# Performance work log

Measured on AMD Instinct MI355X. Metric: run time of the kernel, lower is better.

The kernel has to match this reference:

```python
import jax, jax.numpy as jnp
import numpy as np

THETA = 10000.0

def apply_rope(x, positions):
    # x: [B, H, S, D_head], positions: [S] int
    d = x.shape[-1]
    inv_freq = THETA ** (-jnp.arange(0, d, 2, dtype=jnp.float32) / d)  # [d/2]
    ang = positions.astype(jnp.float32)[:, None] * inv_freq[None, :]   # [S, d/2]
    cos, sin = jnp.cos(ang), jnp.sin(ang)                              # broadcast over B,H
    x1, x2 = x[..., 0::2], x[..., 1::2]
    r1 = x1 * cos - x2 * sin
    r2 = x1 * sin + x2 * cos
    return jnp.stack([r1, r2], axis=-1).reshape(x.shape)


def setup_inputs() -> dict:
    key = jax.random.key(0)
    ks = jax.random.split(key, 5)
    B, S, D = 4, 2048, 1024
    scale = 1.0 / np.sqrt(D)
    return {
        "x": jax.random.normal(ks[0], (B, S, D), dtype=jnp.float32),
        "Wq": jax.random.normal(ks[1], (D, D), dtype=jnp.float32) * scale,
        "Wk": jax.random.normal(ks[2], (D, D), dtype=jnp.float32) * scale,
        "Wv": jax.random.normal(ks[3], (D, D), dtype=jnp.float32) * scale,
        "Wo": jax.random.normal(ks[4], (D, D), dtype=jnp.float32) * scale,
        "token_positions": jnp.arange(S, dtype=jnp.int32),
    }


def reference(x, Wq, Wk, Wv, Wo, token_positions):
    B, S, D = x.shape
    H = 16
    hd = D // H
    # fused QKV projection (weights stored [out, in], y = x @ W^T, no bias)
    qkv_w = jnp.concatenate([Wq, Wk, Wv], axis=0)          # [3D, D]
    qkv = x @ qkv_w.T                                      # [B, S, 3D]
    q, k, v = jnp.split(qkv, 3, axis=-1)
    # [B, S, D] -> [B, H, S, hd]
    def split_heads(t):
        return t.reshape(B, S, H, hd).transpose(0, 2, 1, 3)
    q, k, v = split_heads(q), split_heads(k), split_heads(v)
    q = apply_rope(q, token_positions)
    k = apply_rope(k, token_positions)
    scores = jnp.einsum('bhqd,bhkd->bhqk', q, k) / jnp.sqrt(jnp.float32(hd))
    causal = jnp.tril(jnp.ones((S, S), dtype=bool))        # True = attend
    scores = jnp.where(causal[None, None], scores, -jnp.inf)
    attn = jax.nn.softmax(scores, axis=-1)
    out = jnp.einsum('bhqk,bhkd->bhqd', attn, v)           # [B, H, S, hd]
    out = out.transpose(0, 2, 1, 3).reshape(B, S, D)
    return out @ Wo.T
```

## Files before the change

### kernel.cpp

```cpp
#include <hip/hip_runtime.h>
#include <hip/hip_bf16.h>


typedef __bf16 bf16x8 __attribute__((ext_vector_type(8)));
typedef float f32x4 __attribute__((ext_vector_type(4)));
typedef unsigned short u16x8 __attribute__((ext_vector_type(8)));

#define DEV static __device__ __forceinline__

DEV unsigned short f2bf(float f) {
  unsigned int u = __builtin_bit_cast(unsigned int, f);
  u += 0x7FFFu + ((u >> 16) & 1u);
  return (unsigned short)(u >> 16);
}
DEV float bf2f(unsigned short h) {
  unsigned int u = ((unsigned int)h) << 16;
  return __builtin_bit_cast(float, u);
}
DEV bf16x8 ld_bf8(const unsigned short* p) {
  union { u16x8 u; bf16x8 b; } c;
  c.u = *reinterpret_cast<const u16x8*>(p);
  return c.b;
}
DEV unsigned int pk2(float a, float b) {
  unsigned int r;
  asm("v_cvt_pk_bf16_f32 %0, %1, %2" : "=v"(r) : "v"(a), "v"(b));
  return r;
}

DEV void gload_lds16(const unsigned short* src, unsigned short* dst) {
  __builtin_amdgcn_global_load_lds(
      (const __attribute__((address_space(1))) void*)src,
      (__attribute__((address_space(3))) void*)dst, 16, 0, 0);
}

DEV void stage_tile(const unsigned short* g, int ldg, unsigned short* lds,
                    int wave, int lane) {
  int rl = lane >> 3;
  int c16 = lane & 7;
#pragma unroll
  for (int i = 0; i < 4; ++i) {
    int row = i * 32 + wave * 8 + rl;
    int sc16 = c16 ^ (row & 7);
    const unsigned short* src = g + (size_t)row * ldg + sc16 * 8;
    unsigned short* dst = lds + (i * 32 + wave * 8) * 64;
    gload_lds16(src, dst);
  }
}

DEV bf16x8 lds_frag(const unsigned short* lds, int row, int c16) {
  return ld_bf8(lds + row * 64 + ((c16 ^ (row & 7)) << 3));
}

__global__ void k_f32_to_bf16(const float* __restrict__ in,
                              unsigned short* __restrict__ out, int n4) {
  int i = blockIdx.x * blockDim.x + threadIdx.x;
  if (i < n4) {
    float4 v = reinterpret_cast<const float4*>(in)[i];
    uint2 o;
    o.x = pk2(v.x, v.y);
    o.y = pk2(v.z, v.w);
    reinterpret_cast<uint2*>(out)[i] = o;
  }
}

__global__ void k_conv_w(const float* __restrict__ Wq, const float* __restrict__ Wk,
                         const float* __restrict__ Wv, const float* __restrict__ Wo,
                         unsigned short* __restrict__ Wb, unsigned short* __restrict__ Wob) {
  int i = blockIdx.x * blockDim.x + threadIdx.x;
  int which = i >> 18, j = i & 262143;
  const float* src = (which == 0) ? Wq : (which == 1) ? Wk : (which == 2) ? Wv : Wo;
  unsigned short* dst = (which == 3) ? Wob : Wb + (size_t)which * 1048576;
  float4 v = reinterpret_cast<const float4*>(src)[j];
  uint2 o;
  o.x = pk2(v.x, v.y);
  o.y = pk2(v.z, v.w);
  reinterpret_cast<uint2*>(dst)[j] = o;
}

__global__ void k_rope_table(const int* __restrict__ pos, float* __restrict__ tab) {
  int idx = blockIdx.x * blockDim.x + threadIdx.x;
  if (idx >= 2048 * 32) return;
  int s = idx >> 5, i = idx & 31;
  double inv = pow(10000.0, -(double)(2 * i) / 64.0);
  double ang = (double)pos[s] * inv;
  tab[idx * 2]     = (float)cos(ang);
  tab[idx * 2 + 1] = (float)sin(ang);
}

__global__ __launch_bounds__(256) void k_gemm_qkv(
    const unsigned short* __restrict__ A, const unsigned short* __restrict__ W,
    unsigned short* __restrict__ Qh, unsigned short* __restrict__ Kh,
    unsigned short* __restrict__ Vt, const float* __restrict__ tab) {
  const int Kd = 1024, S = 2048;
  __shared__ __align__(16) unsigned short As[128 * 64];
  __shared__ __align__(16) unsigned short Bs[128 * 64];
  int m0 = blockIdx.x * 128, n0 = blockIdx.y * 128;
  int wave = threadIdx.x >> 6, lane = threadIdx.x & 63;
  int wm = wave >> 1, wn = wave & 1;
  int lr = lane & 15, lk = lane >> 4;
  const unsigned short* Ag = A + (size_t)m0 * Kd;
  const unsigned short* Wg = W + (size_t)n0 * Kd;
  f32x4 acc[4][4] = {};
  for (int k0 = 0; k0 < Kd; k0 += 64) {
    stage_tile(Ag + k0, Kd, As, wave, lane);
    stage_tile(Wg + k0, Kd, Bs, wave, lane);
    __syncthreads();
#pragma unroll
    for (int ks = 0; ks < 2; ++ks) {
      bf16x8 a[4], b[4];
#pragma unroll
      for (int fm = 0; fm < 4; ++fm) a[fm] = lds_frag(As, wm * 64 + fm * 16 + lr, ks * 4 + lk);
#pragma unroll
      for (int fn = 0; fn < 4; ++fn) b[fn] = lds_frag(Bs, wn * 64 + fn * 16 + lr, ks * 4 + lk);
#pragma unroll
      for (int fm = 0; fm < 4; ++fm)
#pragma unroll
        for (int fn = 0; fn < 4; ++fn)
          acc[fm][fn] = __builtin_amdgcn_mfma_f32_16x16x32_bf16(a[fm], b[fn], acc[fm][fn], 0, 0, 0);
    }
    __syncthreads();
  }
  int t = n0 >> 10;
  if (t == 2) {
#pragma unroll
    for (int fm = 0; fm < 4; ++fm) {
      int row = m0 + wm * 64 + fm * 16 + lk * 4;
      int bb = row >> 11, s0 = row & 2047;
#pragma unroll
      for (int fn = 0; fn < 4; ++fn) {
        int col = n0 + wn * 64 + fn * 16 + lr;
        int h = (col >> 6) & 15, d = col & 63;
        uint2 w;
        w.x = pk2(acc[fm][fn][0], acc[fm][fn][1]);
        w.y = pk2(acc[fm][fn][2], acc[fm][fn][3]);
        *reinterpret_cast<uint2*>(Vt + (((size_t)(bb * 16 + h) * 64) + d) * S + s0) = w;
      }
    }
  } else {
    unsigned short* dst0 = (t == 0) ? Qh : Kh;
#pragma unroll
    for (int fm = 0; fm < 4; ++fm) {
      int row = m0 + wm * 64 + fm * 16 + lk * 4;
#pragma unroll
      for (int fn = 0; fn < 4; ++fn) {
        int col = n0 + wn * 64 + fn * 16 + lr;
        int h = (col >> 6) & 15, d = col & 63;
        int ri = d >> 1;
        bool odd = d & 1;
#pragma unroll
        for (int r = 0; r < 4; ++r) {
          int rr = row + r;
          int bb = rr >> 11, s = rr & 2047;
          float2 cs = reinterpret_cast<const float2*>(tab)[s * 32 + ri];
          float v = acc[fm][fn][r];
          float other = __shfl_xor(v, 1);
          float res = odd ? (other * cs.y + v * cs.x)
                          : (v * cs.x - other * cs.y);
          dst0[(((size_t)(bb * 16 + h) * S) + s) * 64 + d] = f2bf(res);
        }
      }
    }
  }
}

__global__ __launch_bounds__(256) void k_attn(
    const unsigned short* __restrict__ Qh, const unsigned short* __restrict__ Kh,
    const unsigned short* __restrict__ Vt, unsigned short* __restrict__ Obuf) {
  const int S = 2048;
  const float KF = 0.18033688f;
  const float RAW_THR = 44.3614f;
  int bh = blockIdx.x;
  int b = bh >> 4, h = bh & 15;
  int wave = threadIdx.x >> 6, lane = threadIdx.x & 63;
  int lr = lane & 15, lk = lane >> 4;
  int qt = (int)gridDim.y - 1 - (int)blockIdx.y;
  int q0 = qt * 128 + wave * 32;
  const unsigned short* Qp = Qh + (size_t)bh * S * 64;
  const unsigned short* Kp = Kh + (size_t)bh * S * 64;
  const unsigned short* Vp = Vt + (size_t)bh * 64 * S;

  __shared__ __align__(16) unsigned short Ks[2][64 * 64];
  __shared__ __align__(16) unsigned short Vs[2][64 * 64];
  __shared__ __align__(16) unsigned short P_all[4][32][64];
  char* pw = (char*)&P_all[wave][0][0];

  auto STAGE = [&](int buf, int kv0) {
    int rl = lane >> 3, c16 = lane & 7;
#pragma unroll
    for (int i = 0; i < 2; ++i) {
      int row = wave * 16 + i * 8 + rl;
      int sc = (c16 ^ (row & 7)) << 3;
      gload_lds16(Kp + (size_t)(kv0 + row) * 64 + sc, &Ks[buf][(wave * 16 + i * 8) * 64]);
      gload_lds16(Vp + (size_t)row * S + kv0 + sc,    &Vs[buf][(wave * 16 + i * 8) * 64]);
    }
  };

  bf16x8 qb[2][2];
#pragma unroll
  for (int mi = 0; mi < 2; ++mi)
#pragma unroll
    for (int ks = 0; ks < 2; ++ks)
      qb[mi][ks] = ld_bf8(Qp + (size_t)(q0 + mi * 16 + lr) * 64 + ks * 32 + lk * 8);

  f32x4 acc_o[4][2] = {};
  float m_run[2] = {-1e30f, -1e30f}, l_run[2] = {0.f, 0.f};
  int my_nt = (q0 + 31) / 64 + 1;
  int NT = 2 * qt + 2;

  STAGE(0, 0);
  __syncthreads();

  for (int t = 0; t < NT; ++t) {
    int cur = t & 1;
    if (t + 1 < NT) STAGE(cur ^ 1, (t + 1) * 64);
    if (t < my_nt) {
      int kv0 = t * 64;
      bf16x8 ka[4][2];
#pragma unroll
      for (int ni = 0; ni < 4; ++ni)
#pragma unroll
        for (int ks = 0; ks < 2; ++ks)
          ka[ni][ks] = lds_frag(&Ks[cur][0], ni * 16 + lr, ks * 4 + lk);
      f32x4 st[4][2] = {};
      __builtin_amdgcn_s_setprio(1);
#pragma unroll
      for (int ni = 0; ni < 4; ++ni)
#pragma unroll
        for (int mi = 0; mi < 2; ++mi) {
          st[ni][mi] = __builtin_amdgcn_mfma_f32_16x16x32_bf16(ka[ni][0], qb[mi][0], st[ni][mi], 0, 0, 0);
          st[ni][mi] = __builtin_amdgcn_mfma_f32_16x16x32_bf16(ka[ni][1], qb[mi][1], st[ni][mi], 0, 0, 0);
        }
      __builtin_amdgcn_s_setprio(0);
      bf16x8 va[4][2];
#pragma unroll
      for (int nf = 0; nf < 4; ++nf)
#pragma unroll
        for (int ks = 0; ks < 2; ++ks)
          va[nf][ks] = lds_frag(&Vs[cur][0], nf * 16 + lr, ks * 4 + lk);

      if (kv0 + 63 > q0) {
#pragma unroll
        for (int mi = 0; mi < 2; ++mi) {
          int row = q0 + mi * 16 + lr;
#pragma unroll
          for (int ni = 0; ni < 4; ++ni)
#pragma unroll
            for (int r = 0; r < 4; ++r)
              if (kv0 + ni * 16 + lk * 4 + r > row) st[ni][mi][r] = -3e38f;
        }
      }
      float mx[2];
#pragma unroll
      for (int mi = 0; mi < 2; ++mi) {
        float a0 = fmaxf(fmaxf(st[0][mi][0], st[0][mi][1]), fmaxf(st[0][mi][2], st[0][mi][3]));
        float a1 = fmaxf(fmaxf(st[1][mi][0], st[1][mi][1]), fmaxf(st[1][mi][2], st[1][mi][3]));
        float a2 = fmaxf(fmaxf(st[2][mi][0], st[2][mi][1]), fmaxf(st[2][mi][2], st[2][mi][3]));
        float a3 = fmaxf(fmaxf(st[3][mi][0], st[3][mi][1]), fmaxf(st[3][mi][2], st[3][mi][3]));
        float m = fmaxf(fmaxf(a0, a1), fmaxf(a2, a3));
        m = fmaxf(m, __shfl_xor(m, 16));
        m = fmaxf(m, __shfl_xor(m, 32));
        mx[mi] = m;
      }
      bool small = (mx[0] <= m_run[0] + RAW_THR) && (mx[1] <= m_run[1] + RAW_THR);
      if (!__all(small)) {
#pragma unroll
        for (int mi = 0; mi < 2; ++mi) {
          float m_new = fmaxf(m_run[mi], mx[mi]);
          float scale = __builtin_amdgcn_exp2f((m_run[mi] - m_new) * KF);
          l_run[mi] *= scale;
          m_run[mi] = m_new;
#pragma unroll
          for (int nf = 0; nf < 4; ++nf)
#pragma unroll
            for (int r = 0; r < 4; ++r) acc_o[nf][mi][r] *= scale;
        }
      }
#pragma unroll
      for (int mi = 0; mi < 2; ++mi) {
        float negh = -m_run[mi] * KF;
        int prow = mi * 16 + lr;
        char* rowp = pw + prow * 128;
        int swz = (lr & 7) << 4;
        float rs = 0.f;
#pragma unroll
        for (int ni = 0; ni < 4; ++ni) {
          float p0 = __builtin_amdgcn_exp2f(fmaf(st[ni][mi][0], KF, negh));
          float p1 = __builtin_amdgcn_exp2f(fmaf(st[ni][mi][1], KF, negh));
          float p2 = __builtin_amdgcn_exp2f(fmaf(st[ni][mi][2], KF, negh));
          float p3 = __builtin_amdgcn_exp2f(fmaf(st[ni][mi][3], KF, negh));
          rs += (p0 + p1) + (p2 + p3);
          uint2 w; w.x = pk2(p0, p1); w.y = pk2(p2, p3);
          *reinterpret_cast<uint2*>(rowp + ((ni * 32 + lk * 8) ^ swz)) = w;
        }
        rs += __shfl_xor(rs, 16);
        rs += __shfl_xor(rs, 32);
        l_run[mi] += rs;
      }
      bf16x8 pb[2][2];
#pragma unroll
      for (int mi = 0; mi < 2; ++mi) {
        int prow = mi * 16 + lr;
        int swz = (lr & 7) << 4;
#pragma unroll
        for (int ks = 0; ks < 2; ++ks)
          pb[mi][ks] = ld_bf8((const unsigned short*)(pw + prow * 128 + ((ks * 64 + lk * 16) ^ swz)));
      }
      __builtin_amdgcn_s_setprio(1);
#pragma unroll
      for (int nf = 0; nf < 4; ++nf)
#pragma unroll
        for (int mi = 0; mi < 2; ++mi) {
          acc_o[nf][mi] = __builtin_amdgcn_mfma_f32_16x16x32_bf16(va[nf][0], pb[mi][0], acc_o[nf][mi], 0, 0, 0);
          acc_o[nf][mi] = __builtin_amdgcn_mfma_f32_16x16x32_bf16(va[nf][1], pb[mi][1], acc_o[nf][mi], 0, 0, 0);
        }
      __builtin_amdgcn_s_setprio(0);
    }
    __syncthreads();
  }

#pragma unroll
  for (int mi = 0; mi < 2; ++mi) {
    float inv_l = 1.f / l_run[mi];
    int q = q0 + mi * 16 + lr;
    size_t base = ((size_t)b * S + q) * 1024 + h * 64;
#pragma unroll
    for (int nf = 0; nf < 4; ++nf) {
      uint2 w;
      w.x = pk2(acc_o[nf][mi][0] * inv_l, acc_o[nf][mi][1] * inv_l);
      w.y = pk2(acc_o[nf][mi][2] * inv_l, acc_o[nf][mi][3] * inv_l);
      *reinterpret_cast<uint2*>(Obuf + base + nf * 16 + lk * 4) = w;
    }
  }
}

__global__ __launch_bounds__(256) void k_gemm_out(
    const unsigned short* __restrict__ A, const unsigned short* __restrict__ W,
    float* __restrict__ C) {
  const int Kd = 1024;
  __shared__ __align__(16) unsigned short As[128 * 64];
  __shared__ __align__(16) unsigned short Bs[128 * 64];
  int m0 = blockIdx.x * 128, n0 = blockIdx.y * 128;
  int wave = threadIdx.x >> 6, lane = threadIdx.x & 63;
  int wm = wave >> 1, wn = wave & 1;
  int lr = lane & 15, lk = lane >> 4;
  const unsigned short* Ag = A + (size_t)m0 * Kd;
  const unsigned short* Wg = W + (size_t)n0 * Kd;
  f32x4 acc[4][4] = {};
  for (int k0 = 0; k0 < Kd; k0 += 64) {
    stage_tile(Ag + k0, Kd, As, wave, lane);
    stage_tile(Wg + k0, Kd, Bs, wave, lane);
    __syncthreads();
#pragma unroll
    for (int ks = 0; ks < 2; ++ks) {
      bf16x8 a[4], b[4];
#pragma unroll
      for (int fm = 0; fm < 4; ++fm) a[fm] = lds_frag(As, wm * 64 + fm * 16 + lr, ks * 4 + lk);
#pragma unroll
      for (int fn = 0; fn < 4; ++fn) b[fn] = lds_frag(Bs, wn * 64 + fn * 16 + lr, ks * 4 + lk);
#pragma unroll
      for (int fm = 0; fm < 4; ++fm)
#pragma unroll
        for (int fn = 0; fn < 4; ++fn)
          acc[fm][fn] = __builtin_amdgcn_mfma_f32_16x16x32_bf16(a[fm], b[fn], acc[fm][fn], 0, 0, 0);
    }
    __syncthreads();
  }
#pragma unroll
  for (int fm = 0; fm < 4; ++fm)
#pragma unroll
    for (int fn = 0; fn < 4; ++fn)
#pragma unroll
      for (int r = 0; r < 4; ++r)
        C[(size_t)(m0 + wm * 64 + fm * 16 + lk * 4 + r) * 1024 + n0 + wn * 64 + fn * 16 + lr] =
            acc[fm][fn][r];
}

extern "C" void kernel_launch(void* const* d_in, const int* in_sizes, int n_in,
                              void* d_out, int out_size, void* d_ws, size_t ws_size,
                              hipStream_t stream) {
  const float* x  = (const float*)d_in[0];
  const float* Wq = (const float*)d_in[1];
  const float* Wk = (const float*)d_in[2];
  const float* Wv = (const float*)d_in[3];
  const float* Wo = (const float*)d_in[4];
  const int* pos  = (const int*)d_in[5];
  float* out = (float*)d_out;
  char* ws = (char*)d_ws;

  unsigned short* xb  = (unsigned short*)(ws);
  unsigned short* Wb  = (unsigned short*)(ws + 16777216);
  unsigned short* Wob = (unsigned short*)(ws + 23068672);
  unsigned short* Qh  = (unsigned short*)(ws + 25165824);
  unsigned short* Kh  = (unsigned short*)(ws + 41943040);
  unsigned short* Ob  = (unsigned short*)(ws + 58720256);
  unsigned short* Vt  = (unsigned short*)(ws + 75497472);
  float* tab          = (float*)(ws + 92274688);
  (void)in_sizes; (void)n_in; (void)out_size; (void)ws_size;

  k_f32_to_bf16<<<8192, 256, 0, stream>>>(x, xb, 2097152);
  k_conv_w<<<4096, 256, 0, stream>>>(Wq, Wk, Wv, Wo, Wb, Wob);
  k_rope_table<<<256, 256, 0, stream>>>(pos, tab);

  dim3 g1(64, 24);
  k_gemm_qkv<<<g1, 256, 0, stream>>>(xb, Wb, Qh, Kh, Vt, tab);
  dim3 ga(64, 16);
  k_attn<<<ga, 256, 0, stream>>>(Qh, Kh, Vt, Ob);
  dim3 g2(64, 8);
  k_gemm_out<<<g2, 256, 0, stream>>>(Ob, Wob, out);
}
```

Baseline: 189.0 us.

## Pair complementary causal query tiles per attention block for load balance

Each attention block now handles two query tiles, qt and 15-qt, so every block does about the same amount of causal work. The K/V tiles staged into shared memory are reused by both query tiles, and the grid is halved from 16 to 8 in y. The trade-off is twice the accumulator and Q-fragment registers, which may lower occupancy. There are also only 512 blocks to spread across the CUs.

```diff
diff --git a/kernel.cpp b/kernel.cpp
--- a/kernel.cpp
+++ b/kernel.cpp
@@ -174,8 +174,10 @@
   int b = bh >> 4, h = bh & 15;
   int wave = threadIdx.x >> 6, lane = threadIdx.x & 63;
   int lr = lane & 15, lk = lane >> 4;
-  int qt = (int)gridDim.y - 1 - (int)blockIdx.y;
-  int q0 = qt * 128 + wave * 32;
+  int qtA = blockIdx.y;
+  int qtB = 15 - qtA;
+  int q0A = qtA * 128 + wave * 32;
+  int q0B = qtB * 128 + wave * 32;
   const unsigned short* Qp = Qh + (size_t)bh * S * 64;
   const unsigned short* Kp = Kh + (size_t)bh * S * 64;
   const unsigned short* Vp = Vt + (size_t)bh * 64 * S;
@@ -196,17 +198,124 @@
     }
   };
 
-  bf16x8 qb[2][2];
+  bf16x8 qbA[2][2], qbB[2][2];
 #pragma unroll
   for (int mi = 0; mi < 2; ++mi)
 #pragma unroll
-    for (int ks = 0; ks < 2; ++ks)
-      qb[mi][ks] = ld_bf8(Qp + (size_t)(q0 + mi * 16 + lr) * 64 + ks * 32 + lk * 8);
-
-  f32x4 acc_o[4][2] = {};
-  float m_run[2] = {-1e30f, -1e30f}, l_run[2] = {0.f, 0.f};
-  int my_nt = (q0 + 31) / 64 + 1;
-  int NT = 2 * qt + 2;
+    for (int ks = 0; ks < 2; ++ks) {
+      qbA[mi][ks] = ld_bf8(Qp + (size_t)(q0A + mi * 16 + lr) * 64 + ks * 32 + lk * 8);
+      qbB[mi][ks] = ld_bf8(Qp + (size_t)(q0B + mi * 16 + lr) * 64 + ks * 32 + lk * 8);
+    }
+
+  f32x4 accA[4][2] = {}, accB[4][2] = {};
+  float mA[2] = {-1e30f, -1e30f}, lA[2] = {0.f, 0.f};
+  float mB[2] = {-1e30f, -1e30f}, lB[2] = {0.f, 0.f};
+  int ntA = (q0A + 31) / 64 + 1;
+  int ntB = (q0B + 31) / 64 + 1;
+  int NT = 2 * qtB + 2;
+
+  auto PROC = [&](int q0, bf16x8 (&qb)[2][2], f32x4 (&acc_o)[4][2],
+                  float (&m_run)[2], float (&l_run)[2], int kv0, int cur) {
+    bf16x8 ka[4][2];
+#pragma unroll
+    for (int ni = 0; ni < 4; ++ni)
+#pragma unroll
+      for (int ks = 0; ks < 2; ++ks)
+        ka[ni][ks] = lds_frag(&Ks[cur][0], ni * 16 + lr, ks * 4 + lk);
+    f32x4 st[4][2] = {};
+    __builtin_amdgcn_s_setprio(1);
+#pragma unroll
+    for (int ni = 0; ni < 4; ++ni)
+#pragma unroll
+      for (int mi = 0; mi < 2; ++mi) {
+        st[ni][mi] = __builtin_amdgcn_mfma_f32_16x16x32_bf16(ka[ni][0], qb[mi][0], st[ni][mi], 0, 0, 0);
+        st[ni][mi] = __builtin_amdgcn_mfma_f32_16x16x32_bf16(ka[ni][1], qb[mi][1], st[ni][mi], 0, 0, 0);
+      }
+    __builtin_amdgcn_s_setprio(0);
+    bf16x8 va[4][2];
+#pragma unroll
+    for (int nf = 0; nf < 4; ++nf)
+#pragma unroll
+      for (int ks = 0; ks < 2; ++ks)
+        va[nf][ks] = lds_frag(&Vs[cur][0], nf * 16 + lr, ks * 4 + lk);
+
+    if (kv0 + 63 > q0) {
+#pragma unroll
+      for (int mi = 0; mi < 2; ++mi) {
+        int row = q0 + mi * 16 + lr;
+#pragma unroll
+        for (int ni = 0; ni < 4; ++ni)
+#pragma unroll
+          for (int r = 0; r < 4; ++r)
+            if (kv0 + ni * 16 + lk * 4 + r > row) st[ni][mi][r] = -3e38f;
+      }
+    }
+    float mx[2];
+#pragma unroll
+    for (int mi = 0; mi < 2; ++mi) {
+      float a0 = fmaxf(fmaxf(st[0][mi][0], st[0][mi][1]), fmaxf(st[0][mi][2], st[0][mi][3]));
+      float a1 = fmaxf(fmaxf(st[1][mi][0], st[1][mi][1]), fmaxf(st[1][mi][2], st[1][mi][3]));
+      float a2 = fmaxf(fmaxf(st[2][mi][0], st[2][mi][1]), fmaxf(st[2][mi][2], st[2][mi][3]));
+      float a3 = fmaxf(fmaxf(st[3][mi][0], st[3][mi][1]), fmaxf(st[3][mi][2], st[3][mi][3]));
+      float m = fmaxf(fmaxf(a0, a1), fmaxf(a2, a3));
+      m = fmaxf(m, __shfl_xor(m, 16));
+      m = fmaxf(m, __shfl_xor(m, 32));
+      mx[mi] = m;
+    }
+    bool small = (mx[0] <= m_run[0] + RAW_THR) && (mx[1] <= m_run[1] + RAW_THR);
+    if (!__all(small)) {
+#pragma unroll
+      for (int mi = 0; mi < 2; ++mi) {
+        float m_new = fmaxf(m_run[mi], mx[mi]);
+        float scale = __builtin_amdgcn_exp2f((m_run[mi] - m_new) * KF);
+        l_run[mi] *= scale;
+        m_run[mi] = m_new;
+#pragma unroll
+        for (int nf = 0; nf < 4; ++nf)
+#pragma unroll
+          for (int r = 0; r < 4; ++r) acc_o[nf][mi][r] *= scale;
+      }
+    }
+#pragma unroll
+    for (int mi = 0; mi < 2; ++mi) {
+      float negh = -m_run[mi] * KF;
+      int prow = mi * 16 + lr;
+      char* rowp = pw + prow * 128;
+      int swz = (lr & 7) << 4;
+      float rs = 0.f;
+#pragma unroll
+      for (int ni = 0; ni < 4; ++ni) {
+        float p0 = __builtin_amdgcn_exp2f(fmaf(st[ni][mi][0], KF, negh));
+        float p1 = __builtin_amdgcn_exp2f(fmaf(st[ni][mi][1], KF, negh));
+        float p2 = __builtin_amdgcn_exp2f(fmaf(st[ni][mi][2], KF, negh));
+        float p3 = __builtin_amdgcn_exp2f(fmaf(st[ni][mi][3], KF, negh));
+        rs += (p0 + p1) + (p2 + p3);
+        uint2 w; w.x = pk2(p0, p1); w.y = pk2(p2, p3);
+        *reinterpret_cast<uint2*>(rowp + ((ni * 32 + lk * 8) ^ swz)) = w;
+      }
+      rs += __shfl_xor(rs, 16);
+      rs += __shfl_xor(rs, 32);
+      l_run[mi] += rs;
+    }
+    bf16x8 pb[2][2];
+#pragma unroll
+    for (int mi = 0; mi < 2; ++mi) {
+      int prow = mi * 16 + lr;
+      int swz = (lr & 7) << 4;
+#pragma unroll
+      for (int ks = 0; ks < 2; ++ks)
+        pb[mi][ks] = ld_bf8((const unsigned short*)(pw + prow * 128 + ((ks * 64 + lk * 16) ^ swz)));
+    }
+    __builtin_amdgcn_s_setprio(1);
+#pragma unroll
+    for (int nf = 0; nf < 4; ++nf)
+#pragma unroll
+      for (int mi = 0; mi < 2; ++mi) {
+        acc_o[nf][mi] = __builtin_amdgcn_mfma_f32_16x16x32_bf16(va[nf][0], pb[mi][0], acc_o[nf][mi], 0, 0, 0);
+        acc_o[nf][mi] = __builtin_amdgcn_mfma_f32_16x16x32_bf16(va[nf][1], pb[mi][1], acc_o[nf][mi], 0, 0, 0);
+      }
+    __builtin_amdgcn_s_setprio(0);
+  };
 
   STAGE(0, 0);
   __syncthreads();
@@ -214,122 +323,28 @@
   for (int t = 0; t < NT; ++t) {
     int cur = t & 1;
     if (t + 1 < NT) STAGE(cur ^ 1, (t + 1) * 64);
-    if (t < my_nt) {
-      int kv0 = t * 64;
-      bf16x8 ka[4][2];
-#pragma unroll
-      for (int ni = 0; ni < 4; ++ni)
-#pragma unroll
-        for (int ks = 0; ks < 2; ++ks)
-          ka[ni][ks] = lds_frag(&Ks[cur][0], ni * 16 + lr, ks * 4 + lk);
-      f32x4 st[4][2] = {};
-      __builtin_amdgcn_s_setprio(1);
-#pragma unroll
-      for (int ni = 0; ni < 4; ++ni)
-#pragma unroll
-        for (int mi = 0; mi < 2; ++mi) {
-          st[ni][mi] = __builtin_amdgcn_mfma_f32_16x16x32_bf16(ka[ni][0], qb[mi][0], st[ni][mi], 0, 0, 0);
-          st[ni][mi] = __builtin_amdgcn_mfma_f32_16x16x32_bf16(ka[ni][1], qb[mi][1], st[ni][mi], 0, 0, 0);
-        }
-      __builtin_amdgcn_s_setprio(0);
-      bf16x8 va[4][2];
-#pragma unroll
-      for (int nf = 0; nf < 4; ++nf)
-#pragma unroll
-        for (int ks = 0; ks < 2; ++ks)
-          va[nf][ks] = lds_frag(&Vs[cur][0], nf * 16 + lr, ks * 4 + lk);
-
-      if (kv0 + 63 > q0) {
-#pragma unroll
-        for (int mi = 0; mi < 2; ++mi) {
-          int row = q0 + mi * 16 + lr;
-#pragma unroll
-          for (int ni = 0; ni < 4; ++ni)
-#pragma unroll
-            for (int r = 0; r < 4; ++r)
-              if (kv0 + ni * 16 + lk * 4 + r > row) st[ni][mi][r] = -3e38f;
-        }
-      }
-      float mx[2];
-#pragma unroll
-      for (int mi = 0; mi < 2; ++mi) {
-        float a0 = fmaxf(fmaxf(st[0][mi][0], st[0][mi][1]), fmaxf(st[0][mi][2], st[0][mi][3]));
-        float a1 = fmaxf(fmaxf(st[1][mi][0], st[1][mi][1]), fmaxf(st[1][mi][2], st[1][mi][3]));
-        float a2 = fmaxf(fmaxf(st[2][mi][0], st[2][mi][1]), fmaxf(st[2][mi][2], st[2][mi][3]));
-        float a3 = fmaxf(fmaxf(st[3][mi][0], st[3][mi][1]), fmaxf(st[3][mi][2], st[3][mi][3]));
-        float m = fmaxf(fmaxf(a0, a1), fmaxf(a2, a3));
-        m = fmaxf(m, __shfl_xor(m, 16));
-        m = fmaxf(m, __shfl_xor(m, 32));
-        mx[mi] = m;
-      }
-      bool small = (mx[0] <= m_run[0] + RAW_THR) && (mx[1] <= m_run[1] + RAW_THR);
-      if (!__all(small)) {
-#pragma unroll
-        for (int mi = 0; mi < 2; ++mi) {
-          float m_new = fmaxf(m_run[mi], mx[mi]);
-          float scale = __builtin_amdgcn_exp2f((m_run[mi] - m_new) * KF);
-          l_run[mi] *= scale;
-          m_run[mi] = m_new;
-#pragma unroll
-          for (int nf = 0; nf < 4; ++nf)
-#pragma unroll
-            for (int r = 0; r < 4; ++r) acc_o[nf][mi][r] *= scale;
-        }
-      }
-#pragma unroll
-      for (int mi = 0; mi < 2; ++mi) {
-        float negh = -m_run[mi] * KF;
-        int prow = mi * 16 + lr;
-        char* rowp = pw + prow * 128;
-        int swz = (lr & 7) << 4;
-        float rs = 0.f;
-#pragma unroll
-        for (int ni = 0; ni < 4; ++ni) {
-          float p0 = __builtin_amdgcn_exp2f(fmaf(st[ni][mi][0], KF, negh));
-          float p1 = __builtin_amdgcn_exp2f(fmaf(st[ni][mi][1], KF, negh));
-          float p2 = __builtin_amdgcn_exp2f(fmaf(st[ni][mi][2], KF, negh));
-          float p3 = __builtin_amdgcn_exp2f(fmaf(st[ni][mi][3], KF, negh));
-          rs += (p0 + p1) + (p2 + p3);
-          uint2 w; w.x = pk2(p0, p1); w.y = pk2(p2, p3);
-          *reinterpret_cast<uint2*>(rowp + ((ni * 32 + lk * 8) ^ swz)) = w;
-        }
-        rs += __shfl_xor(rs, 16);
-        rs += __shfl_xor(rs, 32);
-        l_run[mi] += rs;
-      }
-      bf16x8 pb[2][2];
-#pragma unroll
-      for (int mi = 0; mi < 2; ++mi) {
-        int prow = mi * 16 + lr;
-        int swz = (lr & 7) << 4;
-#pragma unroll
-        for (int ks = 0; ks < 2; ++ks)
-          pb[mi][ks] = ld_bf8((const unsigned short*)(pw + prow * 128 + ((ks * 64 + lk * 16) ^ swz)));
-      }
-      __builtin_amdgcn_s_setprio(1);
-#pragma unroll
-      for (int nf = 0; nf < 4; ++nf)
-#pragma unroll
-        for (int mi = 0; mi < 2; ++mi) {
-          acc_o[nf][mi] = __builtin_amdgcn_mfma_f32_16x16x32_bf16(va[nf][0], pb[mi][0], acc_o[nf][mi], 0, 0, 0);
-          acc_o[nf][mi] = __builtin_amdgcn_mfma_f32_16x16x32_bf16(va[nf][1], pb[mi][1], acc_o[nf][mi], 0, 0, 0);
-        }
-      __builtin_amdgcn_s_setprio(0);
-    }
+    if (t < ntA) PROC(q0A, qbA, accA, mA, lA, t * 64, cur);
+    if (t < ntB) PROC(q0B, qbB, accB, mB, lB, t * 64, cur);
     __syncthreads();
   }
 
 #pragma unroll
-  for (int mi = 0; mi < 2; ++mi) {
-    float inv_l = 1.f / l_run[mi];
-    int q = q0 + mi * 16 + lr;
-    size_t base = ((size_t)b * S + q) * 1024 + h * 64;
-#pragma unroll
-    for (int nf = 0; nf < 4; ++nf) {
-      uint2 w;
-      w.x = pk2(acc_o[nf][mi][0] * inv_l, acc_o[nf][mi][1] * inv_l);
-      w.y = pk2(acc_o[nf][mi][2] * inv_l, acc_o[nf][mi][3] * inv_l);
-      *reinterpret_cast<uint2*>(Obuf + base + nf * 16 + lk * 4) = w;
+  for (int part = 0; part < 2; ++part) {
+    int q0 = part ? q0B : q0A;
+    f32x4(&acc_o)[4][2] = part ? accB : accA;
+    float* l_run = part ? lB : lA;
+#pragma unroll
+    for (int mi = 0; mi < 2; ++mi) {
+      float inv_l = 1.f / l_run[mi];
+      int q = q0 + mi * 16 + lr;
+      size_t base = ((size_t)b * S + q) * 1024 + h * 64;
+#pragma unroll
+      for (int nf = 0; nf < 4; ++nf) {
+        uint2 w;
+        w.x = pk2(acc_o[nf][mi][0] * inv_l, acc_o[nf][mi][1] * inv_l);
+        w.y = pk2(acc_o[nf][mi][2] * inv_l, acc_o[nf][mi][3] * inv_l);
+        *reinterpret_cast<uint2*>(Obuf + base + nf * 16 + lk * 4) = w;
+      }
     }
   }
 }
@@ -404,7 +419,7 @@
 
   dim3 g1(64, 24);
   k_gemm_qkv<<<g1, 256, 0, stream>>>(xb, Wb, Qh, Kh, Vt, tab);
-  dim3 ga(64, 16);
+  dim3 ga(64, 8);
   k_attn<<<ga, 256, 0, stream>>>(Qh, Kh, Vt, Ob);
   dim3 g2(64, 8);
   k_gemm_out<<<g2, 256, 0, stream>>>(Ob, Wob, out);
```

Result: slower. 222.8 us (+17.8%).

## Rewrite QKV GEMM as 8-wave 256x128 tile with triple-buffered direct-to-LDS loads

Applied to the files above, without the earlier changes.

The QKV projection kernel now uses 512 threads computing a 256x128 output tile per block. It triple-buffers A and B tiles in LDS, filled by direct global-to-LDS loads with an XOR swizzle. Loads for step k+2 are issued in two halves interleaved with the MFMA phases, with barriers, vmcnt waits and priority raised around the MFMA bursts. The goal is to hide global memory latency behind compute and halve the reads of W per output, at the cost of much more LDS and tighter scheduling assumptions. The epilogue now derives the Q/K/V region from blockIdx.y.

```diff
diff --git a/kernel.cpp b/kernel.cpp
--- a/kernel.cpp
+++ b/kernel.cpp
@@ -88,41 +88,101 @@
   tab[idx * 2 + 1] = (float)sin(ang);
 }
 
-__global__ __launch_bounds__(256) void k_gemm_qkv(
+__global__ __launch_bounds__(512) void k_gemm_qkv8(
     const unsigned short* __restrict__ A, const unsigned short* __restrict__ W,
     unsigned short* __restrict__ Qh, unsigned short* __restrict__ Kh,
     unsigned short* __restrict__ Vt, const float* __restrict__ tab) {
   const int Kd = 1024, S = 2048;
-  __shared__ __align__(16) unsigned short As[128 * 64];
-  __shared__ __align__(16) unsigned short Bs[128 * 64];
-  int m0 = blockIdx.x * 128, n0 = blockIdx.y * 128;
+  __shared__ __align__(16) unsigned short Asl[3][2][128 * 64];
+  __shared__ __align__(16) unsigned short Bsl[3][128 * 64];
+  int m0 = blockIdx.x * 256, n0 = blockIdx.y * 128;
   int wave = threadIdx.x >> 6, lane = threadIdx.x & 63;
   int wm = wave >> 1, wn = wave & 1;
   int lr = lane & 15, lk = lane >> 4;
-  const unsigned short* Ag = A + (size_t)m0 * Kd;
-  const unsigned short* Wg = W + (size_t)n0 * Kd;
+  int rl = lane >> 3, c16 = lane & 7;
+  int sc16 = c16 ^ rl;
+
+  auto STAGE3 = [&](int sb, int kt, int j0) {
+    int k0 = kt * 64;
+#pragma unroll
+    for (int j = 0; j < 3; ++j) {
+      int c = wave * 6 + j0 + j;
+      if (c < 32) {
+        int half = c >> 4, r0 = (c & 15) * 8;
+        gload_lds16(A + (size_t)(m0 + half * 128 + r0 + rl) * Kd + k0 + sc16 * 8,
+                    &Asl[sb][half][r0 * 64]);
+      } else {
+        int r0 = (c - 32) * 8;
+        gload_lds16(W + (size_t)(n0 + r0 + rl) * Kd + k0 + sc16 * 8,
+                    &Bsl[sb][r0 * 64]);
+      }
+    }
+  };
+
   f32x4 acc[4][4] = {};
-  for (int k0 = 0; k0 < Kd; k0 += 64) {
-    stage_tile(Ag + k0, Kd, As, wave, lane);
-    stage_tile(Wg + k0, Kd, Bs, wave, lane);
-    __syncthreads();
-#pragma unroll
-    for (int ks = 0; ks < 2; ++ks) {
-      bf16x8 a[4], b[4];
-#pragma unroll
-      for (int fm = 0; fm < 4; ++fm) a[fm] = lds_frag(As, wm * 64 + fm * 16 + lr, ks * 4 + lk);
-#pragma unroll
-      for (int fn = 0; fn < 4; ++fn) b[fn] = lds_frag(Bs, wn * 64 + fn * 16 + lr, ks * 4 + lk);
+  bf16x8 afr[4][2];
+
+  STAGE3(0, 0, 0); STAGE3(0, 0, 3);
+  STAGE3(1, 1, 0); STAGE3(1, 1, 3);
+  asm volatile("s_waitcnt vmcnt(0)" ::: "memory");
+  __builtin_amdgcn_sched_barrier(0);
+  __builtin_amdgcn_s_barrier();
+
+  for (int u = 0; u < 16; ++u) {
+    int rb = u % 3, sb = (u + 2) % 3;
+    bool st = (u + 2) < 16;
+#pragma unroll
+    for (int fm = 0; fm < 4; ++fm)
+#pragma unroll
+      for (int ks = 0; ks < 2; ++ks)
+        afr[fm][ks] = lds_frag(&Asl[rb][wm >> 1][0], (wm & 1) * 64 + fm * 16 + lr, ks * 4 + lk);
+    bf16x8 b01[2][2];
+#pragma unroll
+    for (int f = 0; f < 2; ++f)
+#pragma unroll
+      for (int ks = 0; ks < 2; ++ks)
+        b01[f][ks] = lds_frag(&Bsl[rb][0], wn * 64 + f * 16 + lr, ks * 4 + lk);
+    if (st) STAGE3(sb, u + 2, 0);
+    __builtin_amdgcn_s_barrier();
+    asm volatile("s_waitcnt lgkmcnt(0)" ::: "memory");
+    __builtin_amdgcn_sched_barrier(0);
+    __builtin_amdgcn_s_setprio(1);
+#pragma unroll
+    for (int f = 0; f < 2; ++f)
 #pragma unroll
       for (int fm = 0; fm < 4; ++fm)
 #pragma unroll
-        for (int fn = 0; fn < 4; ++fn)
-          acc[fm][fn] = __builtin_amdgcn_mfma_f32_16x16x32_bf16(a[fm], b[fn], acc[fm][fn], 0, 0, 0);
-    }
-    __syncthreads();
-  }
-  int t = n0 >> 10;
-  if (t == 2) {
+        for (int ks = 0; ks < 2; ++ks)
+          acc[fm][f] = __builtin_amdgcn_mfma_f32_16x16x32_bf16(afr[fm][ks], b01[f][ks], acc[fm][f], 0, 0, 0);
+    __builtin_amdgcn_s_setprio(0);
+    __builtin_amdgcn_s_barrier();
+    bf16x8 b23[2][2];
+#pragma unroll
+    for (int f = 0; f < 2; ++f)
+#pragma unroll
+      for (int ks = 0; ks < 2; ++ks)
+        b23[f][ks] = lds_frag(&Bsl[rb][0], wn * 64 + (2 + f) * 16 + lr, ks * 4 + lk);
+    if (st) STAGE3(sb, u + 2, 3);
+    __builtin_amdgcn_s_barrier();
+    asm volatile("s_waitcnt lgkmcnt(0)" ::: "memory");
+    __builtin_amdgcn_sched_barrier(0);
+    __builtin_amdgcn_s_setprio(1);
+#pragma unroll
+    for (int f = 0; f < 2; ++f)
+#pragma unroll
+      for (int fm = 0; fm < 4; ++fm)
+#pragma unroll
+        for (int ks = 0; ks < 2; ++ks)
+          acc[fm][2 + f] = __builtin_amdgcn_mfma_f32_16x16x32_bf16(afr[fm][ks], b23[f][ks], acc[fm][2 + f], 0, 0, 0);
+    __builtin_amdgcn_s_setprio(0);
+    if (u >= 13) asm volatile("s_waitcnt vmcnt(0)" ::: "memory");
+    else         asm volatile("s_waitcnt vmcnt(6)" ::: "memory");
+    __builtin_amdgcn_sched_barrier(0);
+    __builtin_amdgcn_s_barrier();
+  }
+
+  int treg = blockIdx.y >> 3;
+  if (treg == 2) {
 #pragma unroll
     for (int fm = 0; fm < 4; ++fm) {
       int row = m0 + wm * 64 + fm * 16 + lk * 4;
@@ -138,7 +198,7 @@
       }
     }
   } else {
-    unsigned short* dst0 = (t == 0) ? Qh : Kh;
+    unsigned short* dst0 = (treg == 0) ? Qh : Kh;
 #pragma unroll
     for (int fm = 0; fm < 4; ++fm) {
       int row = m0 + wm * 64 + fm * 16 + lk * 4;
@@ -402,8 +462,8 @@
   k_conv_w<<<4096, 256, 0, stream>>>(Wq, Wk, Wv, Wo, Wb, Wob);
   k_rope_table<<<256, 256, 0, stream>>>(pos, tab);
 
-  dim3 g1(64, 24);
-  k_gemm_qkv<<<g1, 256, 0, stream>>>(xb, Wb, Qh, Kh, Vt, tab);
+  dim3 g1(32, 24);
+  k_gemm_qkv8<<<g1, 512, 0, stream>>>(xb, Wb, Qh, Kh, Vt, tab);
   dim3 ga(64, 16);
   k_attn<<<ga, 256, 0, stream>>>(Qh, Kh, Vt, Ob);
   dim3 g2(64, 8);
```

Measured after the change: 188.2 us. No clear change (-0.4%).
